# Kernel optimization log

Hardware: AMD Instinct MI355X
Metric: run time of the kernel (lower is better)

Reference implementation:

```python
import jax, jax.numpy as jnp
import numpy as np
from jax import lax

POOL = 7          # pool_size
SR = 2            # bilinear sampling ratio per bin axis
SCALE = 0.125     # spatial_scale for FPN level p3 (1/8)
NUM_CLASSES = 21
SCORE_T = 0.05
NMS_T = 0.5
MAXDET = 100
LBL_OFF = 1.0e4   # per-class box offset for batched NMS


def setup_inputs() -> dict:
    key = jax.random.key(0)
    ks = jax.random.split(key, 8)
    feature_map = jax.random.normal(ks[0], (256, 100, 100), jnp.float32)
    # proposals: valid xyxy boxes inside an 800x800 image
    xy = jax.random.uniform(ks[1], (1000, 2), jnp.float32, 0.0, 700.0)
    wh = jax.random.uniform(ks[2], (1000, 2), jnp.float32, 16.0, 128.0)
    proposals = jnp.concatenate([xy, xy + wh], axis=1)
    fin = 256 * POOL * POOL
    w1 = jax.random.normal(ks[3], (fin, 1024), jnp.float32) * np.sqrt(2.0 / 1024)
    w2 = jax.random.normal(ks[4], (1024, 1024), jnp.float32) * np.sqrt(2.0 / 1024)
    wc = jax.random.normal(ks[5], (1024, NUM_CLASSES), jnp.float32) * 0.01
    wb = jax.random.normal(ks[6], (1024, NUM_CLASSES * 4), jnp.float32) * 0.001
    return {
        'feature_map': feature_map, 'proposals': proposals,
        'w1': w1, 'b1': jnp.zeros((1024,), jnp.float32),
        'w2': w2, 'b2': jnp.zeros((1024,), jnp.float32),
        'wc': wc, 'bc': jnp.zeros((NUM_CLASSES,), jnp.float32),
        'wb': wb, 'bb': jnp.zeros((NUM_CLASSES * 4,), jnp.float32),
    }


def _roi_align(fm, rois):
    """torchvision roi_align, aligned=True, sampling_ratio=SR. fm:[C,H,W] rois:[N,4] xyxy."""
    C, H, W = fm.shape
    b = rois * SCALE - 0.5  # aligned=True half-pixel shift
    x1, y1 = b[:, 0], b[:, 1]
    bw = (b[:, 2] - b[:, 0]) / POOL
    bh = (b[:, 3] - b[:, 1]) / POOL
    # sample offsets within a roi, in units of bin width: [POOL*SR]
    off = (jnp.arange(POOL, dtype=jnp.float32)[:, None]
           + (jnp.arange(SR, dtype=jnp.float32)[None, :] + 0.5) / SR).reshape(-1)
    X = x1[:, None] + off[None, :] * bw[:, None]  # [N, PS]
    Y = y1[:, None] + off[None, :] * bh[:, None]  # [N, PS]

    def axis_prep(v, size):
        valid = (v >= -1.0) & (v <= size)
        v = jnp.clip(v, 0.0, size - 1.0)
        v0 = jnp.floor(v)
        i0 = v0.astype(jnp.int32)
        i1 = jnp.minimum(i0 + 1, size - 1)
        whi = v - v0
        return i0, i1, 1.0 - whi, whi, valid

    x0, x1i, wx0, wx1, vx = axis_prep(X, W)
    y0, y1i, wy0, wy1, vy = axis_prep(Y, H)

    def gath(yi, xi):
        # outer-product advanced indexing -> [C, N, PS, PS]
        return fm[:, yi[:, :, None], xi[:, None, :]]

    val = ((wy0[:, :, None] * wx0[:, None, :]) * gath(y0, x0)
           + (wy0[:, :, None] * wx1[:, None, :]) * gath(y0, x1i)
           + (wy1[:, :, None] * wx0[:, None, :]) * gath(y1i, x0)
           + (wy1[:, :, None] * wx1[:, None, :]) * gath(y1i, x1i))
    val = val * (vy[:, :, None] & vx[:, None, :]).astype(val.dtype)
    N = rois.shape[0]
    val = val.reshape(C, N, POOL, SR, POOL, SR).mean(axis=(3, 5))  # avg over samples
    return val.transpose(1, 0, 2, 3)  # [N, C, POOL, POOL]


def _decode(deltas, boxes):
    """deltas:[N,K,4], boxes:[N,4] xyxy -> [N,K,4] xyxy."""
    w = boxes[:, 2] - boxes[:, 0]
    h = boxes[:, 3] - boxes[:, 1]
    cx = boxes[:, 0] + 0.5 * w
    cy = boxes[:, 1] + 0.5 * h
    dx, dy, dw, dh = deltas[..., 0], deltas[..., 1], deltas[..., 2], deltas[..., 3]
    pcx = dx * w[:, None] + cx[:, None]
    pcy = dy * h[:, None] + cy[:, None]
    pw = jnp.exp(dw) * w[:, None]
    ph = jnp.exp(dh) * h[:, None]
    return jnp.stack([pcx - 0.5 * pw, pcy - 0.5 * ph,
                      pcx + 0.5 * pw, pcy + 0.5 * ph], axis=-1)


def _iou_one(b, B):
    ix1 = jnp.maximum(b[0], B[:, 0]); iy1 = jnp.maximum(b[1], B[:, 1])
    ix2 = jnp.minimum(b[2], B[:, 2]); iy2 = jnp.minimum(b[3], B[:, 3])
    inter = jnp.clip(ix2 - ix1, 0.0) * jnp.clip(iy2 - iy1, 0.0)
    a = (b[2] - b[0]) * (b[3] - b[1])
    A = (B[:, 2] - B[:, 0]) * (B[:, 3] - B[:, 1])
    return inter / (a + A - inter + 1e-9)


def _forward(feature_map, proposals, w1, b1, w2, b2, wc, bc, wb, bb):
    N = proposals.shape[0]
    pooled = _roi_align(feature_map, proposals).reshape(N, -1)  # [N, 12544]
    x = jax.nn.relu(pooled @ w1 + b1)
    x = jax.nn.relu(x @ w2 + b2)
    cls_logits = x @ wc + bc                 # [N, 21]
    box_deltas = x @ wb + bb                 # [N, 84]
    scores = jax.nn.softmax(cls_logits, axis=1)
    fg_scores = scores[:, 1:]                              # [N, 20] drop background
    fg_deltas = box_deltas.reshape(N, NUM_CLASSES, 4)[:, 1:, :]
    boxes = _decode(fg_deltas, proposals)                  # [N, 20, 4]
    K = NUM_CLASSES - 1
    boxes_f = boxes.reshape(N * K, 4)
    scores_f = fg_scores.reshape(N * K)
    labels_f = jnp.tile(jnp.arange(1, NUM_CLASSES, dtype=jnp.int32), N)
    # score threshold as masking (fixed shapes)
    cand = jnp.where(scores_f > SCORE_T, scores_f, -1.0)
    boxes_off = boxes_f + labels_f.astype(boxes_f.dtype)[:, None] * LBL_OFF

    def step(sw, _):
        i = jnp.argmax(sw)
        s = sw[i]
        iou = _iou_one(boxes_off[i], boxes_off)
        sw = jnp.where(iou > NMS_T, -jnp.inf, sw)  # self-IoU=1 removes i too
        return sw, (i, s)

    _, (keep_idx, keep_sc) = lax.scan(step, cand, None, length=MAXDET)
    valid = keep_sc > SCORE_T
    out_boxes = boxes_f[keep_idx] * valid[:, None].astype(boxes_f.dtype)
    out_scores = jnp.where(valid, keep_sc, 0.0)
    out_labels = jnp.where(valid, labels_f[keep_idx], 0)
    return out_boxes, out_scores, out_labels


def reference(feature_map, proposals, w1, b1, w2, b2, wc, bc, wb, bb):
    return _forward(feature_map, proposals, w1, b1, w2, b2, wc, bc, wb, bb)
```

## Files before the change

kernel.cpp:

```cpp
#include <hip/hip_runtime.h>
#include <math.h>

#define NPROP 1000
#define CCH 256
#define FH 100
#define FW 100
#define POOLSZ 7
#define FEAT 12544
#define HID 1024
#define NCLS 21
#define NHEAD 105
#define NCAND 20000
#define SCORE_T 0.05f
#define NMS_T 0.5f
#define MAXDET 100

typedef _Float16 f16;
typedef __attribute__((ext_vector_type(8))) _Float16 f16x8;
typedef __attribute__((ext_vector_type(4))) float f32x4;

__global__ __launch_bounds__(256) void k_transpose(const float* __restrict__ fm,
                                                   float* __restrict__ fmT) {
    __shared__ float lds[64 * 257];
    int posbase = blockIdx.x * 64;
    int tid = threadIdx.x;
    int cq = tid >> 6;
    int pl = tid & 63;
    int pos = posbase + pl;
    bool pok = pos < FH * FW;
    for (int c0 = 0; c0 < CCH; c0 += 4) {
        int c = c0 + cq;
        float v = pok ? fm[c * (FH * FW) + pos] : 0.f;
        lds[pl * 257 + c] = v;
    }
    __syncthreads();
    for (int p = 0; p < 64; ++p) {
        int pos2 = posbase + p;
        if (pos2 < FH * FW) fmT[(size_t)pos2 * CCH + tid] = lds[p * 257 + tid];
    }
}

__global__ __launch_bounds__(256) void k_roi(const float* __restrict__ fmT,
                                             const float* __restrict__ rois,
                                             float* __restrict__ pooled) {
    int n = blockIdx.x;
    int tid = threadIdx.x;
    __shared__ float wx0[14], wx1[14], wy0[14], wy1[14];
    __shared__ int ix0[14], ix1[14], iy0[14], iy1[14], vx[14], vy[14];
    __shared__ float outb[FEAT];

    if (tid < 28) {
        int axis = tid / 14;
        int j = tid % 14;
        float p0 = rois[n * 4 + axis];
        float p1 = rois[n * 4 + 2 + axis];
        float b0 = p0 * 0.125f - 0.5f;
        float b1 = p1 * 0.125f - 0.5f;
        float bsz = (b1 - b0) / 7.0f;
        int p = j >> 1, s = j & 1;
        float off = (float)p + ((float)s + 0.5f) / 2.0f;
        float v = b0 + off * bsz;
        float size = 100.0f;
        int valid = (v >= -1.0f && v <= size) ? 1 : 0;
        v = fminf(fmaxf(v, 0.0f), size - 1.0f);
        float v0 = floorf(v);
        int i0 = (int)v0;
        int i1 = min(i0 + 1, 99);
        float w1v = v - v0;
        float w0v = 1.0f - w1v;
        if (axis == 0) { ix0[j] = i0 * CCH; ix1[j] = i1 * CCH; wx0[j] = w0v; wx1[j] = w1v; vx[j] = valid; }
        else           { iy0[j] = i0 * (FW * CCH); iy1[j] = i1 * (FW * CCH); wy0[j] = w0v; wy1[j] = w1v; vy[j] = valid; }
    }
    __syncthreads();

    int c = tid;
    for (int py = 0; py < POOLSZ; ++py) {
        for (int px = 0; px < POOLSZ; ++px) {
            float acc = 0.f;
            #pragma unroll
            for (int sy = 0; sy < 2; ++sy) {
                int jy = py * 2 + sy;
                if (!vy[jy]) continue;
                float fy0 = wy0[jy], fy1 = wy1[jy];
                int y0 = iy0[jy], y1 = iy1[jy];
                #pragma unroll
                for (int sx = 0; sx < 2; ++sx) {
                    int jx = px * 2 + sx;
                    if (!vx[jx]) continue;
                    float fx0 = wx0[jx], fx1 = wx1[jx];
                    int x0 = ix0[jx], x1 = ix1[jx];
                    float a00 = fmT[y0 + x0 + c];
                    float a01 = fmT[y0 + x1 + c];
                    float a10 = fmT[y1 + x0 + c];
                    float a11 = fmT[y1 + x1 + c];
                    acc += fy0 * (fx0 * a00 + fx1 * a01) + fy1 * (fx0 * a10 + fx1 * a11);
                }
            }
            outb[c * 49 + py * 7 + px] = acc * 0.25f;
        }
    }
    __syncthreads();
    size_t base = (size_t)n * FEAT;
    for (int o = tid; o < FEAT; o += 256)
        pooled[base + o] = outb[o];
}

__global__ __launch_bounds__(256) void k_gemm_mfma(const float* __restrict__ A,
                                                   const float* __restrict__ B,
                                                   float* __restrict__ P,
                                                   int M, int K, int nt) {
    __shared__ f16 Ah[2][2048], Al[2][2048], Bh[2][2048], Bl[2][2048];
    int tid = threadIdx.x;
    int n0 = blockIdx.x * 64;
    int m0 = blockIdx.y * 64;
    int kz = blockIdx.z;
    int kbase0 = kz * nt * 32;

    int a_row = tid >> 2;
    int a_kq  = tid & 3;
    int b_n   = tid & 63;
    int b_kg  = tid >> 6;

    int wave = tid >> 6, lane = tid & 63;
    int wr = (wave >> 1) * 32, wc = (wave & 1) * 32;
    int lhi = lane >> 4, llo = lane & 15;

    f32x4 accm[2][2] = {};
    f32x4 accc[2][2] = {};

    float aS[8], bS[8];
    const float* Arow = A + (size_t)(m0 + a_row) * K;
    bool arow_ok = (m0 + a_row) < M;

    int a_st = a_kq * 512 + ((a_row ^ a_kq) << 3);
    int b_st = b_kg * 512 + (b_n << 3);
    int a_rd0 = lhi * 512 + (((wr + 0  + llo) ^ lhi) << 3);
    int a_rd1 = lhi * 512 + (((wr + 16 + llo) ^ lhi) << 3);
    int b_rd0 = lhi * 512 + ((wc + 0  + llo) << 3);
    int b_rd1 = lhi * 512 + ((wc + 16 + llo) << 3);

    auto LOAD = [&](int t) {
        int kb = kbase0 + t * 32;
        if (arow_ok) {
            const float* ap = Arow + kb + a_kq * 8;
            float4 v0 = *(const float4*)(ap);
            float4 v1 = *(const float4*)(ap + 4);
            aS[0] = v0.x; aS[1] = v0.y; aS[2] = v0.z; aS[3] = v0.w;
            aS[4] = v1.x; aS[5] = v1.y; aS[6] = v1.z; aS[7] = v1.w;
        } else {
            #pragma unroll
            for (int j = 0; j < 8; ++j) aS[j] = 0.f;
        }
        const float* bp = B + (size_t)(kb + b_kg * 8) * 1024 + n0 + b_n;
        #pragma unroll
        for (int j = 0; j < 8; ++j) bS[j] = bp[(size_t)j * 1024];
    };
    auto STORE = [&](int buf) {
        f16x8 vh, vl;
        #pragma unroll
        for (int j = 0; j < 8; ++j) {
            f16 h = (f16)aS[j];
            vh[j] = h;
            vl[j] = (f16)((aS[j] - (float)h) * 4096.0f);
        }
        *(f16x8*)&Ah[buf][a_st] = vh;
        *(f16x8*)&Al[buf][a_st] = vl;
        #pragma unroll
        for (int j = 0; j < 8; ++j) {
            f16 h = (f16)bS[j];
            vh[j] = h;
            vl[j] = (f16)((bS[j] - (float)h) * 4096.0f);
        }
        *(f16x8*)&Bh[buf][b_st] = vh;
        *(f16x8*)&Bl[buf][b_st] = vl;
    };

    LOAD(0);
    STORE(0);
    __syncthreads();

    for (int t = 0; t < nt; ++t) {
        int cur = t & 1;
        if (t + 1 < nt) LOAD(t + 1);
        {
            f16x8 ah0 = *(f16x8*)&Ah[cur][a_rd0];
            f16x8 ah1 = *(f16x8*)&Ah[cur][a_rd1];
            f16x8 bh0 = *(f16x8*)&Bh[cur][b_rd0];
            f16x8 bh1 = *(f16x8*)&Bh[cur][b_rd1];
            f16x8 al0 = *(f16x8*)&Al[cur][a_rd0];
            f16x8 al1 = *(f16x8*)&Al[cur][a_rd1];
            f16x8 bl0 = *(f16x8*)&Bl[cur][b_rd0];
            f16x8 bl1 = *(f16x8*)&Bl[cur][b_rd1];
            accm[0][0] = __builtin_amdgcn_mfma_f32_16x16x32_f16(ah0, bh0, accm[0][0], 0, 0, 0);
            accm[0][1] = __builtin_amdgcn_mfma_f32_16x16x32_f16(ah0, bh1, accm[0][1], 0, 0, 0);
            accm[1][0] = __builtin_amdgcn_mfma_f32_16x16x32_f16(ah1, bh0, accm[1][0], 0, 0, 0);
            accm[1][1] = __builtin_amdgcn_mfma_f32_16x16x32_f16(ah1, bh1, accm[1][1], 0, 0, 0);
            accc[0][0] = __builtin_amdgcn_mfma_f32_16x16x32_f16(ah0, bl0, accc[0][0], 0, 0, 0);
            accc[0][1] = __builtin_amdgcn_mfma_f32_16x16x32_f16(ah0, bl1, accc[0][1], 0, 0, 0);
            accc[1][0] = __builtin_amdgcn_mfma_f32_16x16x32_f16(ah1, bl0, accc[1][0], 0, 0, 0);
            accc[1][1] = __builtin_amdgcn_mfma_f32_16x16x32_f16(ah1, bl1, accc[1][1], 0, 0, 0);
            accc[0][0] = __builtin_amdgcn_mfma_f32_16x16x32_f16(al0, bh0, accc[0][0], 0, 0, 0);
            accc[0][1] = __builtin_amdgcn_mfma_f32_16x16x32_f16(al0, bh1, accc[0][1], 0, 0, 0);
            accc[1][0] = __builtin_amdgcn_mfma_f32_16x16x32_f16(al1, bh0, accc[1][0], 0, 0, 0);
            accc[1][1] = __builtin_amdgcn_mfma_f32_16x16x32_f16(al1, bh1, accc[1][1], 0, 0, 0);
        }
        if (t + 1 < nt) {
            STORE(cur ^ 1);
            __syncthreads();
        }
    }

    const float inv = 1.0f / 4096.0f;
    #pragma unroll
    for (int mi = 0; mi < 2; ++mi) {
        #pragma unroll
        for (int r = 0; r < 4; ++r) {
            int row = m0 + wr + mi * 16 + lhi * 4 + r;
            if (row < M) {
                #pragma unroll
                for (int ni = 0; ni < 2; ++ni) {
                    int col = n0 + wc + ni * 16 + llo;
                    float v = accm[mi][ni][r] + accc[mi][ni][r] * inv;
                    P[(size_t)kz * 1048576 + (size_t)row * 1024 + col] = v;
                }
            }
        }
    }
}

__global__ __launch_bounds__(256) void k_fuse(const float* __restrict__ P,
                                              const float* __restrict__ bias,
                                              float* __restrict__ out) {
    int t = blockIdx.x * 256 + threadIdx.x;
    float4 p0 = ((const float4*)P)[t];
    float4 p1 = ((const float4*)(P + 1048576))[t];
    float4 b  = ((const float4*)bias)[t & 255];
    float4 v;
    v.x = fmaxf(p0.x + p1.x + b.x, 0.f);
    v.y = fmaxf(p0.y + p1.y + b.y, 0.f);
    v.z = fmaxf(p0.z + p1.z + b.z, 0.f);
    v.w = fmaxf(p0.w + p1.w + b.w, 0.f);
    ((float4*)out)[t] = v;
}

__global__ __launch_bounds__(128) void k_heads(const float* __restrict__ x2,
                                               const float* __restrict__ wc,
                                               const float* __restrict__ bc,
                                               const float* __restrict__ wb,
                                               const float* __restrict__ bb,
                                               float* __restrict__ logits) {
    int r0 = blockIdx.x * 4;
    __shared__ float xs[4][HID];
    for (int i = threadIdx.x; i < 4 * HID; i += 128) {
        int rr = i >> 10, kk = i & 1023;
        xs[rr][kk] = x2[(size_t)(r0 + rr) * HID + kk];
    }
    __syncthreads();
    int j = threadIdx.x;
    if (j < NHEAD) {
        float a0 = 0.f, a1 = 0.f, a2 = 0.f, a3 = 0.f;
        if (j < NCLS) {
            for (int k = 0; k < HID; ++k) {
                float w = wc[k * NCLS + j];
                a0 = fmaf(xs[0][k], w, a0);
                a1 = fmaf(xs[1][k], w, a1);
                a2 = fmaf(xs[2][k], w, a2);
                a3 = fmaf(xs[3][k], w, a3);
            }
            float b = bc[j];
            a0 += b; a1 += b; a2 += b; a3 += b;
        } else {
            int jb = j - NCLS;
            for (int k = 0; k < HID; ++k) {
                float w = wb[k * 84 + jb];
                a0 = fmaf(xs[0][k], w, a0);
                a1 = fmaf(xs[1][k], w, a1);
                a2 = fmaf(xs[2][k], w, a2);
                a3 = fmaf(xs[3][k], w, a3);
            }
            float b = bb[jb];
            a0 += b; a1 += b; a2 += b; a3 += b;
        }
        logits[(size_t)(r0 + 0) * NHEAD + j] = a0;
        logits[(size_t)(r0 + 1) * NHEAD + j] = a1;
        logits[(size_t)(r0 + 2) * NHEAD + j] = a2;
        logits[(size_t)(r0 + 3) * NHEAD + j] = a3;
    }
}

__global__ __launch_bounds__(256) void k_prep(const float* __restrict__ logits,
                                              const float* __restrict__ rois,
                                              float* __restrict__ boxes,
                                              float* __restrict__ cand,
                                              float* __restrict__ boxesT) {
    int n = blockIdx.x * 256 + threadIdx.x;
    if (n >= NPROP) return;
    const float* L = logits + (size_t)n * NHEAD;
    float m = L[0];
    #pragma unroll
    for (int k = 1; k < NCLS; ++k) m = fmaxf(m, L[k]);
    float sum = 0.f;
    #pragma unroll
    for (int k = 0; k < NCLS; ++k) sum += expf(L[k] - m);

    float p0 = rois[n * 4 + 0], p1 = rois[n * 4 + 1];
    float p2 = rois[n * 4 + 2], p3 = rois[n * 4 + 3];
    float w = p2 - p0, h = p3 - p1;
    float cx = p0 + 0.5f * w, cy = p1 + 0.5f * h;

    for (int k = 1; k < NCLS; ++k) {
        int i = n * 20 + (k - 1);
        float s = expf(L[k] - m) / sum;
        const float* D = L + NCLS + k * 4;
        float dx = D[0], dy = D[1], dw = D[2], dh = D[3];
        float pcx = dx * w + cx;
        float pcy = dy * h + cy;
        float pw = expf(dw) * w;
        float ph = expf(dh) * h;
        float b0 = pcx - 0.5f * pw;
        float b1 = pcy - 0.5f * ph;
        float b2 = pcx + 0.5f * pw;
        float b3 = pcy + 0.5f * ph;
        boxes[(size_t)i * 4 + 0] = b0;
        boxes[(size_t)i * 4 + 1] = b1;
        boxes[(size_t)i * 4 + 2] = b2;
        boxes[(size_t)i * 4 + 3] = b3;
        cand[i] = (s > SCORE_T) ? s : -__builtin_inff();
        float offv = (float)k * 10000.0f;
        ((float4*)boxesT)[(k - 1) * 1024 + n] =
            make_float4(b0 + offv, b1 + offv, b2 + offv, b3 + offv);
    }
}

__global__ __launch_bounds__(256) void k_nms_cls(const float* __restrict__ cand,
                                                 const float* __restrict__ boxesT,
                                                 unsigned long long* __restrict__ accG,
                                                 int* __restrict__ accN) {
    __shared__ unsigned long long gkeys[2];
    __shared__ unsigned long long accL[MAXDET];
    __shared__ float sb4[4];
    __shared__ int sM;
    int tid = threadIdx.x;
    int c = blockIdx.x;
    if (tid == 0) { gkeys[0] = 0ULL; gkeys[1] = 0ULL; sM = MAXDET; }

    float s[4];
    float4 bx[4];
    #pragma unroll
    for (int r = 0; r < 4; ++r) {
        int n = tid + (r << 8);
        if (n < NPROP) {
            s[r] = cand[n * 20 + c];
            bx[r] = ((const float4*)boxesT)[c * 1024 + n];
        } else {
            s[r] = -__builtin_inff();
            bx[r] = make_float4(0.f, 0.f, 0.f, 0.f);
        }
    }
    __syncthreads();

    for (int it = 0; it < MAXDET; ++it) {
        int cur = it & 1;
        unsigned long long k = 0ULL;
        #pragma unroll
        for (int r = 0; r < 4; ++r) {
            if (s[r] > 0.0f) {
                int n = tid + (r << 8);
                unsigned long long kk =
                    ((unsigned long long)__float_as_uint(s[r]) << 32) |
                    (unsigned long long)(0xFFFFFFFFu - (unsigned)(n * 20 + c));
                if (kk > k) k = kk;
            }
        }
        #pragma unroll
        for (int off = 32; off > 0; off >>= 1) {
            unsigned long long o = __shfl_down(k, off);
            if (o > k) k = o;
        }
        if ((tid & 63) == 0) atomicMax(&gkeys[cur], k);
        __syncthreads();
        unsigned long long g = gkeys[cur];
        if (tid == 0) {
            gkeys[cur ^ 1] = 0ULL;
            accL[it] = g;
            if (g == 0ULL) sM = it;
        }
        if (g != 0ULL) {
            int n_win = (int)(0xFFFFFFFFu - (unsigned)(g & 0xFFFFFFFFu)) / 20;
            if ((n_win & 255) == tid) {
                float4 b = bx[n_win >> 8];
                sb4[0] = b.x; sb4[1] = b.y; sb4[2] = b.z; sb4[3] = b.w;
            }
        }
        __syncthreads();
        if (g == 0ULL) break;

        float q0 = sb4[0], q1 = sb4[1], q2 = sb4[2], q3 = sb4[3];
        float qa = (q2 - q0) * (q3 - q1);
        #pragma unroll
        for (int r = 0; r < 4; ++r) {
            if (s[r] > 0.0f) {
                float4 cb = bx[r];
                float ix1 = fmaxf(q0, cb.x), iy1 = fmaxf(q1, cb.y);
                float ix2 = fminf(q2, cb.z), iy2 = fminf(q3, cb.w);
                float inter = fmaxf(ix2 - ix1, 0.f) * fmaxf(iy2 - iy1, 0.f);
                float A2 = (cb.z - cb.x) * (cb.w - cb.y);
                float iou = inter / (qa + A2 - inter + 1e-9f);
                if (iou > NMS_T) s[r] = -__builtin_inff();
            }
        }
    }

    __syncthreads();
    int mm = sM;
    if (tid < mm) accG[c * MAXDET + tid] = accL[tid];
    if (tid == 0) accN[c] = mm;
}

__global__ __launch_bounds__(128) void k_nms_merge(const unsigned long long* __restrict__ accG,
                                                   const int* __restrict__ accN,
                                                   const float* __restrict__ boxes,
                                                   float* __restrict__ out) {
    __shared__ unsigned long long picks[MAXDET];
    int tid = threadIdx.x;
    if (tid < 64) {
        int c = tid;
        int cnt = (c < 20) ? accN[c] : 0;
        int ptr = 0;
        unsigned long long key = (cnt > 0) ? accG[c * MAXDET] : 0ULL;
        for (int it = 0; it < MAXDET; ++it) {
            unsigned long long k = key;
            #pragma unroll
            for (int off = 32; off > 0; off >>= 1) {
                unsigned long long o = __shfl_down(k, off);
                if (o > k) k = o;
            }
            unsigned long long g = __shfl(k, 0);
            if (tid == 0) picks[it] = g;
            if (g != 0ULL && key == g) {
                ++ptr;
                key = (ptr < cnt) ? accG[c * MAXDET + ptr] : 0ULL;
            }
        }
    }
    __syncthreads();
    if (tid < MAXDET) {
        unsigned long long g = picks[tid];
        if (g != 0ULL) {
            int bi = (int)(0xFFFFFFFFu - (unsigned)(g & 0xFFFFFFFFu));
            float4 b = ((const float4*)boxes)[bi];
            out[tid * 4 + 0] = b.x; out[tid * 4 + 1] = b.y;
            out[tid * 4 + 2] = b.z; out[tid * 4 + 3] = b.w;
            out[400 + tid] = __uint_as_float((unsigned)(g >> 32));
            out[500 + tid] = (float)(bi - (bi / 20) * 20 + 1);
        } else {
            out[tid * 4 + 0] = 0.f; out[tid * 4 + 1] = 0.f;
            out[tid * 4 + 2] = 0.f; out[tid * 4 + 3] = 0.f;
            out[400 + tid] = 0.f;
            out[500 + tid] = 0.f;
        }
    }
}

extern "C" void kernel_launch(void* const* d_in, const int* in_sizes, int n_in,
                              void* d_out, int out_size, void* d_ws, size_t ws_size,
                              hipStream_t stream) {
    const float* fm   = (const float*)d_in[0];
    const float* rois = (const float*)d_in[1];
    const float* w1   = (const float*)d_in[2];
    const float* b1   = (const float*)d_in[3];
    const float* w2   = (const float*)d_in[4];
    const float* b2   = (const float*)d_in[5];
    const float* wc   = (const float*)d_in[6];
    const float* bc   = (const float*)d_in[7];
    const float* wb   = (const float*)d_in[8];
    const float* bb   = (const float*)d_in[9];
    float* out = (float*)d_out;

    float* ws = (float*)d_ws;
    float* fmT    = ws;
    float* P      = ws;
    float* pooled = fmT + 2560000;
    float* x1     = pooled + 12544000;
    float* x2     = x1 + 1024000;
    float* logits = x2 + 1024000;
    float* boxes  = logits + 105000;
    float* cand   = boxes + 80000;
    float* boxesT = pooled;
    unsigned long long* accG   = (unsigned long long*)(pooled + 131072);
    int* accN                  = (int*)(pooled + 135072);

    k_transpose<<<157, 256, 0, stream>>>(fm, fmT);
    k_roi<<<NPROP, 256, 0, stream>>>(fmT, rois, pooled);
    k_gemm_mfma<<<dim3(16, 16, 2), 256, 0, stream>>>(pooled, w1, P, NPROP, FEAT, 196);
    k_fuse<<<1000, 256, 0, stream>>>(P, b1, x1);
    k_gemm_mfma<<<dim3(16, 16, 2), 256, 0, stream>>>(x1, w2, P, NPROP, HID, 16);
    k_fuse<<<1000, 256, 0, stream>>>(P, b2, x2);
    k_heads<<<250, 128, 0, stream>>>(x2, wc, bc, wb, bb, logits);
    k_prep<<<4, 256, 0, stream>>>(logits, rois, boxes, cand, boxesT);
    k_nms_cls<<<20, 256, 0, stream>>>(cand, boxesT, accG, accN);
    k_nms_merge<<<1, 128, 0, stream>>>(accG, accN, boxes, out);
}
```

Before: 745.5 us.

## Emit split-f16 activations from producers and vectorize ROI channel loads

The ROI-align kernel and the first fuse kernel now write the A operand directly as hi/lo f16 pairs. The GEMM therefore loads pre-split halves instead of converting fp32 to split f16 on every tile, for every N-column block. The ROI kernel also reads four channels per float4 and spreads bins across four thread groups. This removes redundant conversion work and keeps A-operand bytes the same (two f16 equal one f32), though the ROI's strided LDS writes may bank-conflict.

Measured after the change: 683.7 us. -8.3%, faster.

```diff
diff --git a/kernel.cpp b/kernel.cpp
--- a/kernel.cpp
+++ b/kernel.cpp
@@ -42,7 +42,8 @@
 
 __global__ __launch_bounds__(256) void k_roi(const float* __restrict__ fmT,
                                              const float* __restrict__ rois,
-                                             float* __restrict__ pooled) {
+                                             f16* __restrict__ poolh,
+                                             f16* __restrict__ pooll) {
     int n = blockIdx.x;
     int tid = threadIdx.x;
     __shared__ float wx0[14], wx1[14], wy0[14], wy1[14];
@@ -68,44 +69,68 @@
         int i1 = min(i0 + 1, 99);
         float w1v = v - v0;
         float w0v = 1.0f - w1v;
-        if (axis == 0) { ix0[j] = i0 * CCH; ix1[j] = i1 * CCH; wx0[j] = w0v; wx1[j] = w1v; vx[j] = valid; }
-        else           { iy0[j] = i0 * (FW * CCH); iy1[j] = i1 * (FW * CCH); wy0[j] = w0v; wy1[j] = w1v; vy[j] = valid; }
-    }
-    __syncthreads();
-
-    int c = tid;
-    for (int py = 0; py < POOLSZ; ++py) {
-        for (int px = 0; px < POOLSZ; ++px) {
-            float acc = 0.f;
+        if (axis == 0) { ix0[j] = i0 * 64; ix1[j] = i1 * 64; wx0[j] = w0v; wx1[j] = w1v; vx[j] = valid; }
+        else           { iy0[j] = i0 * 6400; iy1[j] = i1 * 6400; wy0[j] = w0v; wy1[j] = w1v; vy[j] = valid; }
+    }
+    __syncthreads();
+
+    int cg = tid & 63;
+    int bo = tid >> 6;
+    const float4* fm4 = (const float4*)fmT;
+    for (int bin = bo; bin < 49; bin += 4) {
+        int py = bin / 7;
+        int px = bin - py * 7;
+        float ax = 0.f, ay = 0.f, az = 0.f, aw = 0.f;
+        #pragma unroll
+        for (int sy = 0; sy < 2; ++sy) {
+            int jy = py * 2 + sy;
+            if (!vy[jy]) continue;
+            float fy0 = wy0[jy], fy1 = wy1[jy];
+            int y0 = iy0[jy], y1 = iy1[jy];
             #pragma unroll
-            for (int sy = 0; sy < 2; ++sy) {
-                int jy = py * 2 + sy;
-                if (!vy[jy]) continue;
-                float fy0 = wy0[jy], fy1 = wy1[jy];
-                int y0 = iy0[jy], y1 = iy1[jy];
-                #pragma unroll
-                for (int sx = 0; sx < 2; ++sx) {
-                    int jx = px * 2 + sx;
-                    if (!vx[jx]) continue;
-                    float fx0 = wx0[jx], fx1 = wx1[jx];
-                    int x0 = ix0[jx], x1 = ix1[jx];
-                    float a00 = fmT[y0 + x0 + c];
-                    float a01 = fmT[y0 + x1 + c];
-                    float a10 = fmT[y1 + x0 + c];
-                    float a11 = fmT[y1 + x1 + c];
-                    acc += fy0 * (fx0 * a00 + fx1 * a01) + fy1 * (fx0 * a10 + fx1 * a11);
-                }
-            }
-            outb[c * 49 + py * 7 + px] = acc * 0.25f;
-        }
-    }
-    __syncthreads();
-    size_t base = (size_t)n * FEAT;
-    for (int o = tid; o < FEAT; o += 256)
-        pooled[base + o] = outb[o];
-}
-
-__global__ __launch_bounds__(256) void k_gemm_mfma(const float* __restrict__ A,
+            for (int sx = 0; sx < 2; ++sx) {
+                int jx = px * 2 + sx;
+                if (!vx[jx]) continue;
+                float fx0 = wx0[jx], fx1 = wx1[jx];
+                int x0 = ix0[jx], x1 = ix1[jx];
+                float4 a00 = fm4[y0 + x0 + cg];
+                float4 a01 = fm4[y0 + x1 + cg];
+                float4 a10 = fm4[y1 + x0 + cg];
+                float4 a11 = fm4[y1 + x1 + cg];
+                ax += fy0 * (fx0 * a00.x + fx1 * a01.x) + fy1 * (fx0 * a10.x + fx1 * a11.x);
+                ay += fy0 * (fx0 * a00.y + fx1 * a01.y) + fy1 * (fx0 * a10.y + fx1 * a11.y);
+                az += fy0 * (fx0 * a00.z + fx1 * a01.z) + fy1 * (fx0 * a10.z + fx1 * a11.z);
+                aw += fy0 * (fx0 * a00.w + fx1 * a01.w) + fy1 * (fx0 * a10.w + fx1 * a11.w);
+            }
+        }
+        int c4 = cg * 4;
+        outb[(c4 + 0) * 49 + bin] = ax * 0.25f;
+        outb[(c4 + 1) * 49 + bin] = ay * 0.25f;
+        outb[(c4 + 2) * 49 + bin] = az * 0.25f;
+        outb[(c4 + 3) * 49 + bin] = aw * 0.25f;
+    }
+    __syncthreads();
+
+    unsigned* ph = (unsigned*)poolh + (size_t)n * 6272;
+    unsigned* pl = (unsigned*)pooll + (size_t)n * 6272;
+    for (int op = tid; op < 6272; op += 256) {
+        float v0 = outb[2 * op];
+        float v1 = outb[2 * op + 1];
+        f16 h0 = (f16)v0;
+        f16 l0 = (f16)((v0 - (float)h0) * 4096.0f);
+        f16 h1 = (f16)v1;
+        f16 l1 = (f16)((v1 - (float)h1) * 4096.0f);
+        unsigned hu = (unsigned)__builtin_bit_cast(unsigned short, h0) |
+                      ((unsigned)__builtin_bit_cast(unsigned short, h1) << 16);
+        unsigned lu = (unsigned)__builtin_bit_cast(unsigned short, l0) |
+                      ((unsigned)__builtin_bit_cast(unsigned short, l1) << 16);
+        ph[op] = hu;
+        pl[op] = lu;
+    }
+}
+
+__global__ __launch_bounds__(256) void k_gemm_mfma(const f16* __restrict__ Ahg,
+                                                   const f16* __restrict__ Alg,
                                                    const float* __restrict__ B,
                                                    float* __restrict__ P,
                                                    int M, int K, int nt) {
@@ -128,9 +153,12 @@
     f32x4 accm[2][2] = {};
     f32x4 accc[2][2] = {};
 
-    float aS[8], bS[8];
-    const float* Arow = A + (size_t)(m0 + a_row) * K;
+    const f16x8 ZERO = {};
+    f16x8 aH = ZERO, aL = ZERO;
+    float bS[8];
     bool arow_ok = (m0 + a_row) < M;
+    const f16* ArowH = Ahg + (size_t)(m0 + a_row) * K;
+    const f16* ArowL = Alg + (size_t)(m0 + a_row) * K;
 
     int a_st = a_kq * 512 + ((a_row ^ a_kq) << 3);
     int b_st = b_kg * 512 + (b_n << 3);
@@ -142,29 +170,19 @@
     auto LOAD = [&](int t) {
         int kb = kbase0 + t * 32;
         if (arow_ok) {
-            const float* ap = Arow + kb + a_kq * 8;
-            float4 v0 = *(const float4*)(ap);
-            float4 v1 = *(const float4*)(ap + 4);
-            aS[0] = v0.x; aS[1] = v0.y; aS[2] = v0.z; aS[3] = v0.w;
-            aS[4] = v1.x; aS[5] = v1.y; aS[6] = v1.z; aS[7] = v1.w;
+            aH = *(const f16x8*)(ArowH + kb + a_kq * 8);
+            aL = *(const f16x8*)(ArowL + kb + a_kq * 8);
         } else {
-            #pragma unroll
-            for (int j = 0; j < 8; ++j) aS[j] = 0.f;
+            aH = ZERO; aL = ZERO;
         }
         const float* bp = B + (size_t)(kb + b_kg * 8) * 1024 + n0 + b_n;
         #pragma unroll
         for (int j = 0; j < 8; ++j) bS[j] = bp[(size_t)j * 1024];
     };
     auto STORE = [&](int buf) {
+        *(f16x8*)&Ah[buf][a_st] = aH;
+        *(f16x8*)&Al[buf][a_st] = aL;
         f16x8 vh, vl;
-        #pragma unroll
-        for (int j = 0; j < 8; ++j) {
-            f16 h = (f16)aS[j];
-            vh[j] = h;
-            vl[j] = (f16)((aS[j] - (float)h) * 4096.0f);
-        }
-        *(f16x8*)&Ah[buf][a_st] = vh;
-        *(f16x8*)&Al[buf][a_st] = vl;
         #pragma unroll
         for (int j = 0; j < 8; ++j) {
             f16 h = (f16)bS[j];
@@ -228,9 +246,9 @@
     }
 }
 
-__global__ __launch_bounds__(256) void k_fuse(const float* __restrict__ P,
-                                              const float* __restrict__ bias,
-                                              float* __restrict__ out) {
+__global__ __launch_bounds__(256) void k_fuse_f32(const float* __restrict__ P,
+                                                  const float* __restrict__ bias,
+                                                  float* __restrict__ out) {
     int t = blockIdx.x * 256 + threadIdx.x;
     float4 p0 = ((const float4*)P)[t];
     float4 p1 = ((const float4*)(P + 1048576))[t];
@@ -241,6 +259,34 @@
     v.z = fmaxf(p0.z + p1.z + b.z, 0.f);
     v.w = fmaxf(p0.w + p1.w + b.w, 0.f);
     ((float4*)out)[t] = v;
+}
+
+__global__ __launch_bounds__(256) void k_fuse_f16(const float* __restrict__ P,
+                                                  const float* __restrict__ bias,
+                                                  f16* __restrict__ oh,
+                                                  f16* __restrict__ ol) {
+    int t = blockIdx.x * 256 + threadIdx.x;
+    float4 p0 = ((const float4*)P)[t];
+    float4 p1 = ((const float4*)(P + 1048576))[t];
+    float4 b  = ((const float4*)bias)[t & 255];
+    float v[4];
+    v[0] = fmaxf(p0.x + p1.x + b.x, 0.f);
+    v[1] = fmaxf(p0.y + p1.y + b.y, 0.f);
+    v[2] = fmaxf(p0.z + p1.z + b.z, 0.f);
+    v[3] = fmaxf(p0.w + p1.w + b.w, 0.f);
+    unsigned hu[4], lu[4];
+    #pragma unroll
+    for (int e = 0; e < 4; ++e) {
+        f16 h = (f16)v[e];
+        f16 l = (f16)((v[e] - (float)h) * 4096.0f);
+        hu[e] = __builtin_bit_cast(unsigned short, h);
+        lu[e] = __builtin_bit_cast(unsigned short, l);
+    }
+    uint2 hp, lp;
+    hp.x = hu[0] | (hu[1] << 16); hp.y = hu[2] | (hu[3] << 16);
+    lp.x = lu[0] | (lu[1] << 16); lp.y = lu[2] | (lu[3] << 16);
+    ((uint2*)oh)[t] = hp;
+    ((uint2*)ol)[t] = lp;
 }
 
 __global__ __launch_bounds__(128) void k_heads(const float* __restrict__ x2,
@@ -480,22 +526,26 @@
     float* ws = (float*)d_ws;
     float* fmT    = ws;
     float* P      = ws;
-    float* pooled = fmT + 2560000;
-    float* x1     = pooled + 12544000;
-    float* x2     = x1 + 1024000;
+    float* poolr  = ws + 2560000;
+    f16*   poolh  = (f16*)poolr;
+    f16*   pooll  = (f16*)(poolr + 6272000);
+    float* x1r    = poolr + 12544000;
+    f16*   x1h    = (f16*)x1r;
+    f16*   x1l    = (f16*)(x1r + 512000);
+    float* x2     = x1r + 1024000;
     float* logits = x2 + 1024000;
     float* boxes  = logits + 105000;
     float* cand   = boxes + 80000;
-    float* boxesT = pooled;
-    unsigned long long* accG   = (unsigned long long*)(pooled + 131072);
-    int* accN                  = (int*)(pooled + 135072);
+    float* boxesT = poolr;
+    unsigned long long* accG   = (unsigned long long*)(poolr + 131072);
+    int* accN                  = (int*)(poolr + 135072);
 
     k_transpose<<<157, 256, 0, stream>>>(fm, fmT);
-    k_roi<<<NPROP, 256, 0, stream>>>(fmT, rois, pooled);
-    k_gemm_mfma<<<dim3(16, 16, 2), 256, 0, stream>>>(pooled, w1, P, NPROP, FEAT, 196);
-    k_fuse<<<1000, 256, 0, stream>>>(P, b1, x1);
-    k_gemm_mfma<<<dim3(16, 16, 2), 256, 0, stream>>>(x1, w2, P, NPROP, HID, 16);
-    k_fuse<<<1000, 256, 0, stream>>>(P, b2, x2);
+    k_roi<<<NPROP, 256, 0, stream>>>(fmT, rois, poolh, pooll);
+    k_gemm_mfma<<<dim3(16, 16, 2), 256, 0, stream>>>(poolh, pooll, w1, P, NPROP, FEAT, 196);
+    k_fuse_f16<<<1000, 256, 0, stream>>>(P, b1, x1h, x1l);
+    k_gemm_mfma<<<dim3(16, 16, 2), 256, 0, stream>>>(x1h, x1l, w2, P, NPROP, HID, 16);
+    k_fuse_f32<<<1000, 256, 0, stream>>>(P, b2, x2);
     k_heads<<<250, 128, 0, stream>>>(x2, wc, bc, wb, bb, logits);
     k_prep<<<4, 256, 0, stream>>>(logits, rois, boxes, cand, boxesT);
     k_nms_cls<<<20, 256, 0, stream>>>(cand, boxesT, accG, accN);
```
